# Optimization experiments

Hardware: AMD Instinct MI355X
Metric: run time of the kernel (lower is better)

Reference implementation:

```python
import jax, jax.numpy as jnp
import numpy as np

N, P, VEC, M = 100000, 96, 4, 70000
GROUPS = [27, 8, 8]
K = sum(GROUPS)  # 43
# Replicates the original's use of the LOCAL per-group offset index i_k when
# selecting attention weights in the output accumulation loop.
ATTN_IDX = np.concatenate([np.arange(g) for g in GROUPS]).astype(np.int32)


def setup_inputs() -> dict:
    key = jax.random.key(0)
    ks = jax.random.split(key, 12)
    rng = np.random.default_rng(0)
    # Kernel maps: per offset, M (in_idx, out_idx) pairs; out indices unique per
    # offset (each output point has at most one neighbor at a given offset).
    kmaps = np.stack([
        np.stack([rng.integers(0, N, M), rng.permutation(N)[:M]], axis=1)
        for _ in range(K)
    ]).astype(np.int32)  # [K, M, 2]
    w = lambda k, shape: jax.random.normal(k, shape, jnp.float32) * 0.05
    return dict(
        x=w(ks[0], (N, P)),
        coords=jax.random.uniform(ks[1], (N, 3), jnp.float32, 0.0, 100.0),
        Wq1=w(ks[2], (27, P, P)), gq1=jnp.ones(P), bq1=jnp.zeros(P),
        Wq2=w(ks[3], (27, P, VEC)), gq2=jnp.ones(VEC), bq2=jnp.zeros(VEC),
        Wv=w(ks[4], (27, P, P)), gv=jnp.ones(P), bv=jnp.zeros(P),
        Wp1=w(ks[5], (3, P)), gp1=jnp.ones(P), bp1=jnp.zeros(P),
        Wp2=w(ks[6], (P, VEC)), gp2=jnp.ones(VEC), bp2=jnp.zeros(VEC),
        W1=w(ks[7], (VEC, P)), b1=jnp.zeros(P),
        W2=w(ks[8], (P, VEC)), b2=jnp.zeros(VEC),
        g_out=jnp.ones(P), b_out=jnp.zeros(P),
        kmaps=jnp.asarray(kmaps),
    )


def _bn(x, g, b, eps=1e-5):
    m = x.mean(0)
    v = x.var(0)
    return g * (x - m) * jax.lax.rsqrt(v + eps) + b


def _sparse_conv3(x, W, km27, n):
    # Minkowski kernel-size-3 sparse conv: out[dst] += x[src] @ W[k] per offset.
    def step(acc, kw):
        km, Wk = kw
        return acc.at[km[:, 1]].add(x[km[:, 0]] @ Wk), None
    out, _ = jax.lax.scan(step, jnp.zeros((n, W.shape[-1]), x.dtype), (km27, W))
    return out


def _cbr(x, W, g, b, km27, n):
    return jax.nn.relu(_bn(_sparse_conv3(x, W, km27, n), g, b))


def _forward(x, coords, Wq1, gq1, bq1, Wq2, gq2, bq2, Wv, gv, bv,
             Wp1, gp1, bp1, Wp2, gp2, bp2, W1, b1, W2, b2, g_out, b_out, kmaps):
    n, p = x.shape
    rep = p // VEC  # expand_vec_dim factor
    km27 = kmaps[:27]
    # q branch: two conv3-BN-ReLU stages -> [N, VEC]
    qf = _cbr(_cbr(x, Wq1, gq1, bq1, km27, n), Wq2, gq2, bq2, km27, n)
    # v branch: conv3-BN-ReLU -> [N, P]
    vf = _cbr(x, Wv, gv, bv, km27, n)
    # positional encoding: two 1x1 conv-BN-ReLU on coords -> [N, VEC] -> [N, P]
    pe = jax.nn.relu(_bn(jax.nn.relu(_bn(coords @ Wp1, gp1, bp1)) @ Wp2, gp2, bp2))
    v_f = vf + jnp.repeat(pe, rep, axis=1)

    def attn_step(carry, km):
        src, dst = km[:, 0], km[:, 1]
        # presence mask of offset-k neighbors (scatter of x features, zero elsewhere)
        sm = jnp.zeros((n, p), x.dtype).at[dst].set(x[src])
        mask = jax.lax.stop_gradient((jnp.abs(sm).sum(-1) > 0).astype(x.dtype))  # [N]
        gq = jnp.zeros((n, VEC), x.dtype).at[dst].set(qf[src])
        d = gq - qf * mask[:, None]
        logits = (jax.nn.relu(d @ W1 + b1) @ W2 + b2) * mask[:, None]
        return carry, (logits, mask)

    _, (logits, masks) = jax.lax.scan(attn_step, None, kmaps)  # [K,N,VEC], [K,N]
    attn = jax.nn.softmax(logits, axis=0)  # softmax across the K stacked offsets
    attn_sel = attn[jnp.asarray(ATTN_IDX)]  # replicate local-index selection bug

    def out_step(acc, inp):
        km, mask, a = inp
        nv = jnp.zeros((n, p), x.dtype).at[km[:, 1]].set(v_f[km[:, 0]]) * mask[:, None]
        return acc + nv * jnp.repeat(a, rep, axis=1), None

    out, _ = jax.lax.scan(out_step, jnp.zeros((n, p), x.dtype),
                          (kmaps, masks, attn_sel))
    # out BN + ReLU, residual (inplanes == planes so res = x)
    return jax.nn.relu(_bn(out, g_out, b_out)) + x


def reference(x, coords, Wq1, gq1, bq1, Wq2, gq2, bq2, Wv, gv, bv,
              Wp1, gp1, bp1, Wp2, gp2, bp2, W1, b1, W2, b2, g_out, b_out, kmaps):
    return _forward(x, coords, Wq1, gq1, bq1, Wq2, gq2, bq2, Wv, gv, bv,
                    Wp1, gp1, bp1, Wp2, gp2, bp2, W1, b1, W2, b2,
                    g_out, b_out, kmaps)
```

## Files before the change

### kernel.cpp

```cpp
#include <hip/hip_runtime.h>
#include <math.h>

#define N_  100000
#define P_  96
#define V_  4
#define M_  70000
#define K_  43
#define KC_ 27

typedef unsigned short u16;
typedef __attribute__((ext_vector_type(8))) short bf16x8;
typedef __attribute__((ext_vector_type(4))) float f32x4;
typedef __attribute__((ext_vector_type(16))) float f32x16;

__device__ __forceinline__ u16 f2bf(float f) {
    unsigned int u = __float_as_uint(f);
    u += 0x7fffu + ((u >> 16) & 1u);
    return (u16)(u >> 16);
}
__device__ __forceinline__ float bf2f(u16 h) {
    return __uint_as_float(((unsigned int)h) << 16);
}

__device__ __forceinline__ void gl_lds16(const u16* g, u16* l) {
    __builtin_amdgcn_global_load_lds(
        (const __attribute__((address_space(1))) void*)g,
        (__attribute__((address_space(3))) void*)l, 16, 0, 0);
}

__global__ __launch_bounds__(256) void k_build_srcof(const int* __restrict__ km,
                                                     int* __restrict__ srcOf) {
    int idx = blockIdx.x * 256 + threadIdx.x;
    if (idx >= K_ * M_) return;
    int k = idx / M_;
    int e = idx - k * M_;
    const int* p = km + (size_t)(k * M_ + e) * 2;
    srcOf[(size_t)k * N_ + p[1]] = p[0];
}

__global__ __launch_bounds__(256) void k_rowabs_cvt(const float* __restrict__ x,
                                                    float* __restrict__ rowAbs,
                                                    u16* __restrict__ xb) {
    int row = blockIdx.x * 4 + (threadIdx.x >> 6);
    int lane = threadIdx.x & 63;
    if (row >= N_) return;
    const float* xr = x + (size_t)row * 96;
    float s = 0.f;
    for (int j = lane; j < 96; j += 64) {
        float v = xr[j];
        s += fabsf(v);
        xb[(size_t)row * 96 + j] = f2bf(v);
    }
#pragma unroll
    for (int o = 32; o > 0; o >>= 1) s += __shfl_down(s, o, 64);
    if (lane == 0) rowAbs[row] = s;
}

__global__ __launch_bounds__(256) void k_wt96p(const float* __restrict__ W,
                                               u16* __restrict__ Wp) {
    int idx = blockIdx.x * 256 + threadIdx.x;
    if (idx >= KC_ * 96 * 96) return;
    int k = idx / 9216, rem = idx - k * 9216, n = rem / 96, j = rem - n * 96;
    Wp[(size_t)k * 10240 + n * 104 + j] = f2bf(W[(size_t)k * 9216 + j * 96 + n]);
}

__global__ __launch_bounds__(256) void k_wt4(const float* __restrict__ W,
                                             u16* __restrict__ Wt) {
    int idx = blockIdx.x * 256 + threadIdx.x;
    if (idx >= KC_ * 16 * 96) return;
    int k = idx / 1536, rem = idx - k * 1536, n = rem / 96, j = rem - n * 96;
    Wt[idx] = (n < 4) ? f2bf(W[(size_t)k * 384 + j * 4 + n]) : (u16)0;
}

__global__ __launch_bounds__(256) void k_w12b(const float* __restrict__ W1,
                                              const float* __restrict__ W2,
                                              u16* __restrict__ w1b,
                                              u16* __restrict__ w2b) {
    int t = blockIdx.x * 256 + threadIdx.x;
    if (t < 96 * 32) {
        int j = t >> 5, c = t & 31;
        w1b[t] = (c < 4) ? f2bf(W1[c * 96 + j]) : (u16)0;
    }
    if (t < 16 * 96) {
        int n = t / 96, j = t - n * 96;
        w2b[t] = (n < 4) ? f2bf(W2[j * 4 + n]) : (u16)0;
    }
}

__global__ __launch_bounds__(384, 3) void k_conv96_dual(
    const u16* __restrict__ xb, const u16* __restrict__ Wqp,
    const u16* __restrict__ Wvp, const int* __restrict__ srcOf,
    u16* __restrict__ yQ, u16* __restrict__ yV,
    float* __restrict__ statsQ, float* __restrict__ statsV) {
    __shared__ u16 sA[192 * 104];
    __shared__ u16 sBq[10240];
    __shared__ u16 sBv[10240];
    const int r0 = blockIdx.x * 192;
    const int t = threadIdx.x;
    const int wv = t / 64, lane = t & 63;
    const int n32 = lane & 31, half = lane >> 5;
    const int ea = t >> 1, jca = (t & 1) * 6;
    f32x16 accq[3], accv[3];
#pragma unroll
    for (int i = 0; i < 3; i++) {
#pragma unroll
        for (int j = 0; j < 16; j++) { accq[i][j] = 0.f; accv[i][j] = 0.f; }
    }

    for (int k = 0; k < KC_; k++) {
        __syncthreads();
        {
            const u16* gq = Wqp + (size_t)k * 10240;
            const u16* gv = Wvp + (size_t)k * 10240;
            for (int i = wv; i < 40; i += 6) {
                int mv = (i >= 20);
                int off = (mv ? i - 20 : i) * 512 + lane * 8;
                gl_lds16((mv ? gv : gq) + off, (mv ? (u16*)sBv : (u16*)sBq) + off);
            }
        }
        {
            int r = r0 + ea;
            int src = (r < N_) ? srcOf[(size_t)k * N_ + r] : -1;
            if (src >= 0) {
                const uint4* sp = (const uint4*)(xb + (size_t)src * 96);
#pragma unroll
                for (int i = 0; i < 6; i++)
                    *(uint4*)(sA + ea * 104 + (jca + i) * 8) = sp[jca + i];
            } else {
                uint4 z = make_uint4(0, 0, 0, 0);
#pragma unroll
                for (int i = 0; i < 6; i++)
                    *(uint4*)(sA + ea * 104 + (jca + i) * 8) = z;
            }
        }
        __syncthreads();
#pragma unroll
        for (int ks = 0; ks < 6; ks++) {
            bf16x8 af = *(const bf16x8*)(sA + (wv * 32 + n32) * 104 + ks * 16 + half * 8);
#pragma unroll
            for (int nt = 0; nt < 3; nt++) {
                bf16x8 bq = *(const bf16x8*)(sBq + (nt * 32 + n32) * 104 + ks * 16 + half * 8);
                accq[nt] = __builtin_amdgcn_mfma_f32_32x32x16_bf16(af, bq, accq[nt], 0, 0, 0);
                bf16x8 bv = *(const bf16x8*)(sBv + (nt * 32 + n32) * 104 + ks * 16 + half * 8);
                accv[nt] = __builtin_amdgcn_mfma_f32_32x32x16_bf16(af, bv, accv[nt], 0, 0, 0);
            }
        }
    }
#pragma unroll
    for (int nt = 0; nt < 3; nt++) {
#pragma unroll
        for (int reg = 0; reg < 16; reg++) {
            int row = (reg & 3) + 8 * (reg >> 2) + 4 * half;
            int r = r0 + wv * 32 + row;
            if (r < N_) {
                yQ[(size_t)r * 96 + nt * 32 + n32] = f2bf(accq[nt][reg]);
                yV[(size_t)r * 96 + nt * 32 + n32] = f2bf(accv[nt][reg]);
            }
        }
    }
    __syncthreads();
    float* sred = (float*)sA;
    for (int pass = 0; pass < 2; pass++) {
        f32x16* acc = pass ? accv : accq;
        float* st = pass ? statsV : statsQ;
#pragma unroll
        for (int nt = 0; nt < 3; nt++) {
            float sv = 0.f, qv = 0.f;
#pragma unroll
            for (int reg = 0; reg < 16; reg++) {
                float a = acc[nt][reg];
                sv += a; qv += a * a;
            }
            sv += __shfl_xor(sv, 32, 64);
            qv += __shfl_xor(qv, 32, 64);
            if (half == 0) {
                sred[wv * 192 + nt * 32 + n32] = sv;
                sred[wv * 192 + 96 + nt * 32 + n32] = qv;
            }
        }
        __syncthreads();
        if (t < 192) {
            float tot = 0.f;
#pragma unroll
            for (int w = 0; w < 6; w++) tot += sred[w * 192 + t];
            atomicAdd(&st[t], tot);
        }
        __syncthreads();
    }
}

__global__ __launch_bounds__(256) void k_conv4_mfma(
    const u16* __restrict__ xbA, const u16* __restrict__ Wt4,
    const int* __restrict__ srcOf, float* __restrict__ qf) {
    __shared__ u16 sA[128 * 104];
    __shared__ u16 sB[16 * 104];
    const int r0 = blockIdx.x * 128;
    const int t = threadIdx.x;
    const int wv = t >> 6, lane = t & 63;
    const int m = lane & 15, quad = lane >> 4;
    const int ea = t >> 1, jca = (t & 1) * 6;
    f32x4 acc[2];
    acc[0] = (f32x4){0.f, 0.f, 0.f, 0.f};
    acc[1] = (f32x4){0.f, 0.f, 0.f, 0.f};
    for (int k = 0; k < KC_; k++) {
        __syncthreads();
        {
            int r = r0 + ea;
            int src = (r < N_) ? srcOf[(size_t)k * N_ + r] : -1;
            if (src >= 0) {
                const uint4* sp = (const uint4*)(xbA + (size_t)src * 96);
#pragma unroll
                for (int i = 0; i < 6; i++)
                    *(uint4*)(sA + ea * 104 + (jca + i) * 8) = sp[jca + i];
            } else {
                uint4 z = make_uint4(0, 0, 0, 0);
#pragma unroll
                for (int i = 0; i < 6; i++)
                    *(uint4*)(sA + ea * 104 + (jca + i) * 8) = z;
            }
        }
        if (t < 192) {
            int n = t / 12, jc = t - (t / 12) * 12;
            *(uint4*)(sB + n * 104 + jc * 8) =
                *(const uint4*)(Wt4 + (size_t)k * 1536 + n * 96 + jc * 8);
        }
        __syncthreads();
#pragma unroll
        for (int kk = 0; kk < 3; kk++) {
            bf16x8 bfr = *(const bf16x8*)(sB + m * 104 + kk * 32 + quad * 8);
#pragma unroll
            for (int rt = 0; rt < 2; rt++) {
                bf16x8 af = *(const bf16x8*)(sA + ((wv * 2 + rt) * 16 + m) * 104 + kk * 32 + quad * 8);
                acc[rt] = __builtin_amdgcn_mfma_f32_16x16x32_bf16(af, bfr, acc[rt], 0, 0, 0);
            }
        }
    }
    if (m < 4) {
#pragma unroll
        for (int rt = 0; rt < 2; rt++)
#pragma unroll
            for (int rg = 0; rg < 4; rg++) {
                int r = r0 + (wv * 2 + rt) * 16 + quad * 4 + rg;
                if (r < N_) qf[(size_t)r * 4 + m] = acc[rt][rg];
            }
    }
}

__global__ __launch_bounds__(192) void k_bnstats96(const float* __restrict__ xin,
                                                   float* __restrict__ stats) {
    __shared__ float sS[192], sQ[192];
    int t = threadIdx.x;
    int ch = t % 96, half = t / 96;
    float s = 0.f, q = 0.f;
    for (int r = blockIdx.x * 2 + half; r < N_; r += gridDim.x * 2) {
        float v = xin[(size_t)r * 96 + ch];
        s += v; q += v * v;
    }
    sS[t] = s; sQ[t] = q;
    __syncthreads();
    if (t < 96) {
        atomicAdd(&stats[ch], sS[t] + sS[t + 96]);
        atomicAdd(&stats[96 + ch], sQ[t] + sQ[t + 96]);
    }
}

__global__ __launch_bounds__(256) void k_bnstats4(const float* __restrict__ xin,
                                                  float* __restrict__ stats) {
    __shared__ float sS[256], sQ[256];
    int t = threadIdx.x;
    int c = t & 3, sub = t >> 2;
    float s = 0.f, q = 0.f;
    for (int r = blockIdx.x * 64 + sub; r < N_; r += gridDim.x * 64) {
        float v = xin[(size_t)r * 4 + c];
        s += v; q += v * v;
    }
    sS[t] = s; sQ[t] = q;
    __syncthreads();
    for (int off = 128; off >= 4; off >>= 1) {
        if (t < off) { sS[t] += sS[t + off]; sQ[t] += sQ[t + off]; }
        __syncthreads();
    }
    if (t < 4) {
        atomicAdd(&stats[t], sS[t]);
        atomicAdd(&stats[96 + t], sQ[t]);
    }
}

template <int C, int MODE>
__global__ __launch_bounds__(256) void k_bnapply(float* __restrict__ y,
                                                 const float* __restrict__ stats,
                                                 const float* __restrict__ g,
                                                 const float* __restrict__ b,
                                                 const float* __restrict__ aux) {
    int idx = blockIdx.x * 256 + threadIdx.x;
    if (idx >= N_ * C) return;
    int ch = idx % C;
    float mean = stats[ch] * (1.f / N_);
    float var = stats[96 + ch] * (1.f / N_) - mean * mean;
    float scale = g[ch] * rsqrtf(fmaxf(var, 0.f) + 1e-5f);
    float v = (y[idx] - mean) * scale + b[ch];
    v = fmaxf(v, 0.f);
    if (MODE == 2) v += aux[idx];
    y[idx] = v;
}

template <int MODE>
__global__ __launch_bounds__(256) void k_bnapply96_b2b(
    const u16* __restrict__ yin, const float* __restrict__ stats,
    const float* __restrict__ g, const float* __restrict__ b,
    const float* __restrict__ aux, u16* __restrict__ yout) {
    int idx = blockIdx.x * 256 + threadIdx.x;
    if (idx >= N_ * 96) return;
    int ch = idx % 96;
    float mean = stats[ch] * (1.f / N_);
    float var = stats[96 + ch] * (1.f / N_) - mean * mean;
    float scale = g[ch] * rsqrtf(fmaxf(var, 0.f) + 1e-5f);
    float v = (bf2f(yin[idx]) - mean) * scale + b[ch];
    v = fmaxf(v, 0.f);
    if (MODE == 1) { int r = idx / 96; v += aux[(size_t)r * 4 + (ch / 24)]; }
    yout[idx] = f2bf(v);
}

__global__ __launch_bounds__(256) void k_pe1(const float* __restrict__ coords,
                                             const float* __restrict__ Wp1,
                                             float* __restrict__ out) {
    int idx = blockIdx.x * 256 + threadIdx.x;
    if (idx >= N_ * 96) return;
    int r = idx / 96, ch = idx - r * 96;
    float c0 = coords[r * 3], c1 = coords[r * 3 + 1], c2 = coords[r * 3 + 2];
    out[idx] = c0 * Wp1[ch] + c1 * Wp1[96 + ch] + c2 * Wp1[192 + ch];
}

__global__ __launch_bounds__(256) void k_pe2(const float* __restrict__ hin,
                                             const float* __restrict__ Wp2,
                                             float* __restrict__ out) {
    int idx = blockIdx.x * 256 + threadIdx.x;
    if (idx >= N_ * 4) return;
    int r = idx / 4, c = idx & 3;
    const float* hr = hin + (size_t)r * 96;
    float acc = 0.f;
#pragma unroll 4
    for (int j = 0; j < 96; j++) acc += hr[j] * Wp2[j * 4 + c];
    out[idx] = acc;
}

__global__ __launch_bounds__(256) void k_attn_logits_mfma(
    const float* __restrict__ qf, const int* __restrict__ srcOf,
    const float* __restrict__ rowAbs,
    const u16* __restrict__ w1b, const float* __restrict__ b1,
    const u16* __restrict__ w2b, const float* __restrict__ b2,
    u16* __restrict__ wb) {
    __shared__ u16 hbuf[4][16 * 104];
    __shared__ u16 slogb[32][176];
    __shared__ u16 smk16[32][44];
    const int t = threadIdx.x;
    const int wv = t >> 6, lane = t & 63;
    const int col = lane & 15, quad = lane >> 4;
    const int r0 = blockIdx.x * 32;

    bf16x8 w1f[6];
    float b1v[6];
#pragma unroll
    for (int nt = 0; nt < 6; nt++) {
        w1f[nt] = *(const bf16x8*)(w1b + (nt * 16 + col) * 32 + quad * 8);
        b1v[nt] = b1[nt * 16 + col];
    }
    bf16x8 w2f[3];
#pragma unroll
    for (int kk = 0; kk < 3; kk++)
        w2f[kk] = *(const bf16x8*)(w2b + col * 96 + kk * 32 + quad * 8);
    float b2v = b2[col & 3];

    u16* hb = hbuf[wv];
    for (int tt = 0; tt < 22; tt++) {
        int tileBase = (wv * 22 + tt) * 16;
        bf16x8 af = (bf16x8){0, 0, 0, 0, 0, 0, 0, 0};
        if (quad == 0) {
            int P = tileBase + col;
            int rL = P / 44, k = P - rL * 44;
            int kc = (k < 43) ? k : 42;
            int r = r0 + rL;
            int s = srcOf[(size_t)kc * N_ + r];
            if (k == 43) s = -1;
            int sc = (s >= 0) ? s : 0;
            float mk = (s >= 0 && rowAbs[sc] > 0.f) ? 1.f : 0.f;
            float4 qs = *(const float4*)(qf + (size_t)sc * 4);
            float4 qr = *(const float4*)(qf + (size_t)r * 4);
            af[0] = (short)f2bf((qs.x - qr.x) * mk);
            af[1] = (short)f2bf((qs.y - qr.y) * mk);
            af[2] = (short)f2bf((qs.z - qr.z) * mk);
            af[3] = (short)f2bf((qs.w - qr.w) * mk);
            if (k < 43) smk16[rL][k] = (u16)(mk > 0.f ? 1 : 0);
        }
        f32x4 c1[6];
#pragma unroll
        for (int nt = 0; nt < 6; nt++) {
            c1[nt] = (f32x4){0.f, 0.f, 0.f, 0.f};
            c1[nt] = __builtin_amdgcn_mfma_f32_16x16x32_bf16(af, w1f[nt], c1[nt], 0, 0, 0);
        }
#pragma unroll
        for (int nt = 0; nt < 6; nt++) {
#pragma unroll
            for (int rg = 0; rg < 4; rg++) {
                float h = fmaxf(c1[nt][rg] + b1v[nt], 0.f);
                hb[(quad * 4 + rg) * 104 + nt * 16 + col] = f2bf(h);
            }
        }
        f32x4 acc2 = (f32x4){0.f, 0.f, 0.f, 0.f};
#pragma unroll
        for (int kk = 0; kk < 3; kk++) {
            bf16x8 a2 = *(const bf16x8*)(hb + col * 104 + kk * 32 + quad * 8);
            acc2 = __builtin_amdgcn_mfma_f32_16x16x32_bf16(a2, w2f[kk], acc2, 0, 0, 0);
        }
        if (col < 4) {
#pragma unroll
            for (int rg = 0; rg < 4; rg++) {
                int P = tileBase + quad * 4 + rg;
                int rL = P / 44, k = P - rL * 44;
                if (k < 43) {
                    float mval = (float)smk16[rL][k];
                    slogb[rL][k * 4 + col] = f2bf((acc2[rg] + b2v) * mval);
                }
            }
        }
    }
    __syncthreads();

    if (t < 128) {
        int rL = t >> 2, c = t & 3;
        float mx = 0.f;
        for (int k = 0; k < K_; k++) mx = fmaxf(mx, bf2f(slogb[rL][k * 4 + c]));
        float den = 0.f;
        for (int k = 0; k < K_; k++) den += __expf(bf2f(slogb[rL][k * 4 + c]) - mx);
        float inv = 1.f / den;
        for (int k = 0; k < K_; k++)
            slogb[rL][k * 4 + c] = f2bf(__expf(bf2f(slogb[rL][k * 4 + c]) - mx) * inv);
    }
    __syncthreads();

    for (int p = t; p < 32 * 43; p += 256) {
        int rL = p / 43, k = p - rL * 43;
        int idxk = (k < 27) ? k : ((k < 35) ? (k - 27) : (k - 35));
        u16 mk = smk16[rL][k];
        ushort4 wout = make_ushort4(0, 0, 0, 0);
        if (mk) {
            wout.x = slogb[rL][idxk * 4 + 0];
            wout.y = slogb[rL][idxk * 4 + 1];
            wout.z = slogb[rL][idxk * 4 + 2];
            wout.w = slogb[rL][idxk * 4 + 3];
        }
        *(ushort4*)(wb + ((size_t)(r0 + rL) * 44 + k) * 4) = wout;
    }
}

__global__ __launch_bounds__(256) void k_attn_gather(
    const u16* __restrict__ vfb, const u16* __restrict__ wb,
    const int* __restrict__ srcOf, float* __restrict__ out) {
    int idx = blockIdx.x * 256 + threadIdx.x;
    int r = idx / 24, c4 = idx - r * 24;
    if (r >= N_) return;
    int cg = c4 / 6;
    const u16* wrow = wb + (size_t)r * 176 + cg;
    float a0 = 0.f, a1 = 0.f, a2 = 0.f, a3 = 0.f;
    for (int k = 0; k < K_; k++) {
        int s = srcOf[(size_t)k * N_ + r];
        float w = bf2f(wrow[(size_t)k * 4]);
        w = (s >= 0) ? w : 0.f;
        int sc = (s >= 0) ? s : 0;
        ushort4 v = *(const ushort4*)(vfb + (size_t)sc * 96 + c4 * 4);
        a0 += w * bf2f(v.x);
        a1 += w * bf2f(v.y);
        a2 += w * bf2f(v.z);
        a3 += w * bf2f(v.w);
    }
    *(float4*)(out + (size_t)r * 96 + c4 * 4) = make_float4(a0, a1, a2, a3);
}

extern "C" void kernel_launch(void* const* d_in, const int* in_sizes, int n_in,
                              void* d_out, int out_size, void* d_ws, size_t ws_size,
                              hipStream_t stream) {
    const float* x      = (const float*)d_in[0];
    const float* coords = (const float*)d_in[1];
    const float* Wq1 = (const float*)d_in[2];
    const float* gq1 = (const float*)d_in[3];
    const float* bq1 = (const float*)d_in[4];
    const float* Wq2 = (const float*)d_in[5];
    const float* gq2 = (const float*)d_in[6];
    const float* bq2 = (const float*)d_in[7];
    const float* Wv  = (const float*)d_in[8];
    const float* gv  = (const float*)d_in[9];
    const float* bv  = (const float*)d_in[10];
    const float* Wp1 = (const float*)d_in[11];
    const float* gp1 = (const float*)d_in[12];
    const float* bp1 = (const float*)d_in[13];
    const float* Wp2 = (const float*)d_in[14];
    const float* gp2 = (const float*)d_in[15];
    const float* bp2 = (const float*)d_in[16];
    const float* W1  = (const float*)d_in[17];
    const float* b1  = (const float*)d_in[18];
    const float* W2  = (const float*)d_in[19];
    const float* b2  = (const float*)d_in[20];
    const float* g_out = (const float*)d_in[21];
    const float* b_out = (const float*)d_in[22];
    const int* kmaps = (const int*)d_in[23];
    float* out = (float*)d_out;

    char* ws = (char*)d_ws;
    int*   srcOf  = (int*)ws;
    float* rowAbs = (float*)(ws + 17200000);
    u16*   xb     = (u16*)(ws + 17600000);
    u16*   bufQb  = (u16*)(ws + 36800000);
    u16*   bufVb  = (u16*)(ws + 56000000);
    u16*   bufAb  = (u16*)(ws + 75200000);
    u16*   vfb    = (u16*)(ws + 75200000);
    float* pescr  = (float*)(ws + 17600000);
    u16*   wbuf   = (u16*)(ws + 17600000);
    float* qf     = (float*)(ws + 94400000);
    float* peb    = (float*)(ws + 96000000);
    u16*   Wq1p   = (u16*)(ws + 97600000);
    u16*   Wvp    = (u16*)(ws + 98152960);
    u16*   Wq2t   = (u16*)(ws + 98705920);
    u16*   w1b    = (u16*)(ws + 98788864);
    u16*   w2b    = (u16*)(ws + 98795008);
    float* stats  = (float*)(ws + 98798080);

    hipMemsetAsync(srcOf, 0xFF, (size_t)K_ * N_ * 4, stream);
    hipMemsetAsync(stats, 0, 6 * 192 * 4, stream);

    k_build_srcof<<<(K_ * M_ + 255) / 256, 256, 0, stream>>>(kmaps, srcOf);
    k_rowabs_cvt<<<N_ / 4, 256, 0, stream>>>(x, rowAbs, xb);
    k_wt96p<<<(KC_ * 9216 + 255) / 256, 256, 0, stream>>>(Wq1, Wq1p);
    k_wt96p<<<(KC_ * 9216 + 255) / 256, 256, 0, stream>>>(Wv, Wvp);
    k_wt4<<<(KC_ * 1536 + 255) / 256, 256, 0, stream>>>(Wq2, Wq2t);
    k_w12b<<<12, 256, 0, stream>>>(W1, W2, w1b, w2b);

    const int cbD  = (N_ + 191) / 192;
    const int cb4  = (N_ + 127) / 128;
    const int eb96 = N_ * 96 / 256;
    const int eb4  = (N_ * 4 + 255) / 256;

    k_conv96_dual<<<cbD, 384, 0, stream>>>(xb, Wq1p, Wvp, srcOf, bufQb, bufVb,
                                           stats + 0 * 192, stats + 4 * 192);

    k_bnapply96_b2b<0><<<eb96, 256, 0, stream>>>(bufQb, stats + 0 * 192, gq1, bq1, nullptr, bufAb);
    k_conv4_mfma<<<cb4, 256, 0, stream>>>(bufAb, Wq2t, srcOf, qf);
    k_bnstats4<<<512, 256, 0, stream>>>(qf, stats + 1 * 192);
    k_bnapply<4, 0><<<eb4, 256, 0, stream>>>(qf, stats + 1 * 192, gq2, bq2, nullptr);

    k_pe1<<<eb96, 256, 0, stream>>>(coords, Wp1, pescr);
    k_bnstats96<<<512, 192, 0, stream>>>(pescr, stats + 2 * 192);
    k_bnapply<96, 0><<<eb96, 256, 0, stream>>>(pescr, stats + 2 * 192, gp1, bp1, nullptr);
    k_pe2<<<eb4, 256, 0, stream>>>(pescr, Wp2, peb);
    k_bnstats4<<<512, 256, 0, stream>>>(peb, stats + 3 * 192);
    k_bnapply<4, 0><<<eb4, 256, 0, stream>>>(peb, stats + 3 * 192, gp2, bp2, nullptr);

    k_bnapply96_b2b<1><<<eb96, 256, 0, stream>>>(bufVb, stats + 4 * 192, gv, bv, peb, vfb);

    k_attn_logits_mfma<<<N_ / 32, 256, 0, stream>>>(qf, srcOf, rowAbs, w1b, b1, w2b, b2, wbuf);
    k_attn_gather<<<(N_ * 24) / 256, 256, 0, stream>>>(vfb, wbuf, srcOf, out);

    k_bnstats96<<<512, 192, 0, stream>>>(out, stats + 5 * 192);
    k_bnapply<96, 2><<<eb96, 256, 0, stream>>>(out, stats + 5 * 192, g_out, b_out, x);
}
```

Before: 1.003 ms.

## Reorder q2 conv as per-point projection then gather; fuse BN stats into producers

The second q conv (96->4 over 27 offsets) becomes a dense projection of every point onto all 27 offset weight slices, computed once with MFMA. A lightweight gather kernel then sums the projected values for each point's neighbours, so the full 96-channel rows are no longer gathered 27 times. The BN-apply before that conv is fused into the projection's load. The positional-encoding BN stats move into the pe1 producer, pe1 BN-apply moves into pe2, and the output BN stats are accumulated inside the attention gather kernel, removing separate stats passes. The trade-offs are an extra 108-wide bf16 intermediate buffer, the projection now being rounded to bf16, and more shared/global atomics.

New measurement: 1.096 ms. 9.2% more time.

```diff
diff --git a/kernel.cpp b/kernel.cpp
--- a/kernel.cpp
+++ b/kernel.cpp
@@ -64,12 +64,17 @@
     Wp[(size_t)k * 10240 + n * 104 + j] = f2bf(W[(size_t)k * 9216 + j * 96 + n]);
 }
 
-__global__ __launch_bounds__(256) void k_wt4(const float* __restrict__ W,
-                                             u16* __restrict__ Wt) {
+__global__ __launch_bounds__(256) void k_wtB(const float* __restrict__ W,
+                                             u16* __restrict__ Bimg) {
     int idx = blockIdx.x * 256 + threadIdx.x;
-    if (idx >= KC_ * 16 * 96) return;
-    int k = idx / 1536, rem = idx - k * 1536, n = rem / 96, j = rem - n * 96;
-    Wt[idx] = (n < 4) ? f2bf(W[(size_t)k * 384 + j * 4 + n]) : (u16)0;
+    if (idx >= 128 * 104) return;
+    int n = idx / 104, j = idx - n * 104;
+    u16 v = 0;
+    if (j < 96 && n < 108) {
+        int ks = n >> 2, c = n & 3;
+        v = f2bf(W[(size_t)ks * 384 + j * 4 + c]);
+    }
+    Bimg[idx] = v;
 }
 
 __global__ __launch_bounds__(256) void k_w12b(const float* __restrict__ W1,
@@ -189,79 +194,88 @@
     }
 }
 
-__global__ __launch_bounds__(256) void k_conv4_mfma(
-    const u16* __restrict__ xbA, const u16* __restrict__ Wt4,
-    const int* __restrict__ srcOf, float* __restrict__ qf) {
+__global__ __launch_bounds__(256) void k_proj(
+    const u16* __restrict__ xq, const float* __restrict__ stats,
+    const float* __restrict__ gg, const float* __restrict__ bb,
+    const u16* __restrict__ Bimg, u16* __restrict__ gout) {
     __shared__ u16 sA[128 * 104];
-    __shared__ u16 sB[16 * 104];
+    __shared__ u16 sB[128 * 104];
+    __shared__ float sSc[96], sSh[96];
     const int r0 = blockIdx.x * 128;
     const int t = threadIdx.x;
     const int wv = t >> 6, lane = t & 63;
-    const int m = lane & 15, quad = lane >> 4;
-    const int ea = t >> 1, jca = (t & 1) * 6;
-    f32x4 acc[2];
-    acc[0] = (f32x4){0.f, 0.f, 0.f, 0.f};
-    acc[1] = (f32x4){0.f, 0.f, 0.f, 0.f};
+    const int n32 = lane & 31, half = lane >> 5;
+    if (t < 96) {
+        float mean = stats[t] * (1.f / N_);
+        float var = stats[96 + t] * (1.f / N_) - mean * mean;
+        float sc = gg[t] * rsqrtf(fmaxf(var, 0.f) + 1e-5f);
+        sSc[t] = sc; sSh[t] = bb[t] - mean * sc;
+    }
+    for (int i = t; i < 1664; i += 256)
+        ((uint4*)sB)[i] = ((const uint4*)Bimg)[i];
+    __syncthreads();
+    {
+        int ea = t >> 1, jca = (t & 1) * 6;
+        int r = r0 + ea;
+        bool ok = (r < N_);
+        const u16* xr = xq + (size_t)(ok ? r : 0) * 96;
+#pragma unroll
+        for (int i = 0; i < 6; i++) {
+            int cb = (jca + i) * 8;
+            uint4 v = ok ? *(const uint4*)(xr + cb) : make_uint4(0, 0, 0, 0);
+            const u16* pv = (const u16*)&v;
+            u16 o[8];
+#pragma unroll
+            for (int e = 0; e < 8; e++) {
+                float h = bf2f(pv[e]);
+                h = fmaxf(h * sSc[cb + e] + sSh[cb + e], 0.f);
+                o[e] = f2bf(h);
+            }
+            *(uint4*)(sA + ea * 104 + cb) = *(uint4*)o;
+        }
+    }
+    __syncthreads();
+    f32x16 acc[4];
+#pragma unroll
+    for (int i = 0; i < 4; i++)
+#pragma unroll
+        for (int j = 0; j < 16; j++) acc[i][j] = 0.f;
+#pragma unroll
+    for (int ks = 0; ks < 6; ks++) {
+        bf16x8 af = *(const bf16x8*)(sA + (wv * 32 + n32) * 104 + ks * 16 + half * 8);
+#pragma unroll
+        for (int nt = 0; nt < 4; nt++) {
+            bf16x8 bf = *(const bf16x8*)(sB + (nt * 32 + n32) * 104 + ks * 16 + half * 8);
+            acc[nt] = __builtin_amdgcn_mfma_f32_32x32x16_bf16(af, bf, acc[nt], 0, 0, 0);
+        }
+    }
+#pragma unroll
+    for (int nt = 0; nt < 4; nt++) {
+        int col = nt * 32 + n32;
+        if (col < 108) {
+#pragma unroll
+            for (int reg = 0; reg < 16; reg++) {
+                int row = (reg & 3) + 8 * (reg >> 2) + 4 * half;
+                int r = r0 + wv * 32 + row;
+                if (r < N_) gout[(size_t)r * 108 + col] = f2bf(acc[nt][reg]);
+            }
+        }
+    }
+}
+
+__global__ __launch_bounds__(256) void k_gather4(
+    const u16* __restrict__ g, const int* __restrict__ srcOf,
+    float* __restrict__ qf) {
+    int idx = blockIdx.x * 256 + threadIdx.x;
+    if (idx >= N_ * 4) return;
+    int r = idx >> 2, c = idx & 3;
+    float a = 0.f;
+#pragma unroll
     for (int k = 0; k < KC_; k++) {
-        __syncthreads();
-        {
-            int r = r0 + ea;
-            int src = (r < N_) ? srcOf[(size_t)k * N_ + r] : -1;
-            if (src >= 0) {
-                const uint4* sp = (const uint4*)(xbA + (size_t)src * 96);
-#pragma unroll
-                for (int i = 0; i < 6; i++)
-                    *(uint4*)(sA + ea * 104 + (jca + i) * 8) = sp[jca + i];
-            } else {
-                uint4 z = make_uint4(0, 0, 0, 0);
-#pragma unroll
-                for (int i = 0; i < 6; i++)
-                    *(uint4*)(sA + ea * 104 + (jca + i) * 8) = z;
-            }
-        }
-        if (t < 192) {
-            int n = t / 12, jc = t - (t / 12) * 12;
-            *(uint4*)(sB + n * 104 + jc * 8) =
-                *(const uint4*)(Wt4 + (size_t)k * 1536 + n * 96 + jc * 8);
-        }
-        __syncthreads();
-#pragma unroll
-        for (int kk = 0; kk < 3; kk++) {
-            bf16x8 bfr = *(const bf16x8*)(sB + m * 104 + kk * 32 + quad * 8);
-#pragma unroll
-            for (int rt = 0; rt < 2; rt++) {
-                bf16x8 af = *(const bf16x8*)(sA + ((wv * 2 + rt) * 16 + m) * 104 + kk * 32 + quad * 8);
-                acc[rt] = __builtin_amdgcn_mfma_f32_16x16x32_bf16(af, bfr, acc[rt], 0, 0, 0);
-            }
-        }
-    }
-    if (m < 4) {
-#pragma unroll
-        for (int rt = 0; rt < 2; rt++)
-#pragma unroll
-            for (int rg = 0; rg < 4; rg++) {
-                int r = r0 + (wv * 2 + rt) * 16 + quad * 4 + rg;
-                if (r < N_) qf[(size_t)r * 4 + m] = acc[rt][rg];
-            }
-    }
-}
-
-__global__ __launch_bounds__(192) void k_bnstats96(const float* __restrict__ xin,
-                                                   float* __restrict__ stats) {
-    __shared__ float sS[192], sQ[192];
-    int t = threadIdx.x;
-    int ch = t % 96, half = t / 96;
-    float s = 0.f, q = 0.f;
-    for (int r = blockIdx.x * 2 + half; r < N_; r += gridDim.x * 2) {
-        float v = xin[(size_t)r * 96 + ch];
-        s += v; q += v * v;
-    }
-    sS[t] = s; sQ[t] = q;
-    __syncthreads();
-    if (t < 96) {
-        atomicAdd(&stats[ch], sS[t] + sS[t + 96]);
-        atomicAdd(&stats[96 + ch], sQ[t] + sQ[t + 96]);
-    }
+        int s = srcOf[(size_t)k * N_ + r];
+        if (s >= 0) a += bf2f(g[(size_t)s * 108 + k * 4 + c]);
+    }
+    qf[idx] = a;
 }
 
 __global__ __launch_bounds__(256) void k_bnstats4(const float* __restrict__ xin,
@@ -304,8 +318,7 @@
     y[idx] = v;
 }
 
-template <int MODE>
-__global__ __launch_bounds__(256) void k_bnapply96_b2b(
+__global__ __launch_bounds__(256) void k_bnapply96_pe(
     const u16* __restrict__ yin, const float* __restrict__ stats,
     const float* __restrict__ g, const float* __restrict__ b,
     const float* __restrict__ aux, u16* __restrict__ yout) {
@@ -317,30 +330,60 @@
     float scale = g[ch] * rsqrtf(fmaxf(var, 0.f) + 1e-5f);
     float v = (bf2f(yin[idx]) - mean) * scale + b[ch];
     v = fmaxf(v, 0.f);
-    if (MODE == 1) { int r = idx / 96; v += aux[(size_t)r * 4 + (ch / 24)]; }
+    int r = idx / 96;
+    v += aux[(size_t)r * 4 + (ch / 24)];
     yout[idx] = f2bf(v);
 }
 
-__global__ __launch_bounds__(256) void k_pe1(const float* __restrict__ coords,
-                                             const float* __restrict__ Wp1,
-                                             float* __restrict__ out) {
-    int idx = blockIdx.x * 256 + threadIdx.x;
-    if (idx >= N_ * 96) return;
-    int r = idx / 96, ch = idx - r * 96;
-    float c0 = coords[r * 3], c1 = coords[r * 3 + 1], c2 = coords[r * 3 + 2];
-    out[idx] = c0 * Wp1[ch] + c1 * Wp1[96 + ch] + c2 * Wp1[192 + ch];
-}
-
-__global__ __launch_bounds__(256) void k_pe2(const float* __restrict__ hin,
-                                             const float* __restrict__ Wp2,
-                                             float* __restrict__ out) {
-    int idx = blockIdx.x * 256 + threadIdx.x;
+__global__ __launch_bounds__(192) void k_pe1s(const float* __restrict__ coords,
+                                              const float* __restrict__ Wp1,
+                                              u16* __restrict__ out,
+                                              float* __restrict__ stats) {
+    __shared__ float sS[192], sQ[192];
+    int t = threadIdx.x;
+    int ch = t % 96, half = t / 96;
+    float w0 = Wp1[ch], w1 = Wp1[96 + ch], w2 = Wp1[192 + ch];
+    float s = 0.f, q = 0.f;
+    for (int r = blockIdx.x * 2 + half; r < N_; r += gridDim.x * 2) {
+        float c0 = coords[r * 3], c1 = coords[r * 3 + 1], c2 = coords[r * 3 + 2];
+        float v = c0 * w0 + c1 * w1 + c2 * w2;
+        out[(size_t)r * 96 + ch] = f2bf(v);
+        s += v; q += v * v;
+    }
+    sS[t] = s; sQ[t] = q;
+    __syncthreads();
+    if (t < 96) {
+        atomicAdd(&stats[ch], sS[t] + sS[t + 96]);
+        atomicAdd(&stats[96 + ch], sQ[t] + sQ[t + 96]);
+    }
+}
+
+__global__ __launch_bounds__(256) void k_pe2b(const u16* __restrict__ hin,
+                                              const float* __restrict__ stats,
+                                              const float* __restrict__ gp,
+                                              const float* __restrict__ bp,
+                                              const float* __restrict__ Wp2,
+                                              float* __restrict__ out) {
+    __shared__ float sSc[96], sSh[96], sW[384];
+    int t = threadIdx.x;
+    if (t < 96) {
+        float mean = stats[t] * (1.f / N_);
+        float var = stats[96 + t] * (1.f / N_) - mean * mean;
+        float sc = gp[t] * rsqrtf(fmaxf(var, 0.f) + 1e-5f);
+        sSc[t] = sc; sSh[t] = bp[t] - mean * sc;
+    }
+    for (int i = t; i < 384; i += 256) sW[i] = Wp2[i];
+    __syncthreads();
+    int idx = blockIdx.x * 256 + t;
     if (idx >= N_ * 4) return;
-    int r = idx / 4, c = idx & 3;
-    const float* hr = hin + (size_t)r * 96;
+    int r = idx >> 2, c = idx & 3;
+    const u16* hr = hin + (size_t)r * 96;
     float acc = 0.f;
 #pragma unroll 4
-    for (int j = 0; j < 96; j++) acc += hr[j] * Wp2[j * 4 + c];
+    for (int j = 0; j < 96; j++) {
+        float h = fmaxf(bf2f(hr[j]) * sSc[j] + sSh[j], 0.f);
+        acc += h * sW[j * 4 + c];
+    }
     out[idx] = acc;
 }
 
@@ -453,12 +496,16 @@
     }
 }
 
-__global__ __launch_bounds__(256) void k_attn_gather(
+__global__ __launch_bounds__(256) void k_attn_gather_s(
     const u16* __restrict__ vfb, const u16* __restrict__ wb,
-    const int* __restrict__ srcOf, float* __restrict__ out) {
-    int idx = blockIdx.x * 256 + threadIdx.x;
+    const int* __restrict__ srcOf, float* __restrict__ out,
+    float* __restrict__ stats) {
+    __shared__ float sS[96], sQ[96];
+    int t = threadIdx.x;
+    if (t < 96) { sS[t] = 0.f; sQ[t] = 0.f; }
+    __syncthreads();
+    int idx = blockIdx.x * 256 + t;
     int r = idx / 24, c4 = idx - r * 24;
-    if (r >= N_) return;
     int cg = c4 / 6;
     const u16* wrow = wb + (size_t)r * 176 + cg;
     float a0 = 0.f, a1 = 0.f, a2 = 0.f, a3 = 0.f;
@@ -474,6 +521,16 @@
         a3 += w * bf2f(v.w);
     }
     *(float4*)(out + (size_t)r * 96 + c4 * 4) = make_float4(a0, a1, a2, a3);
+    int chb = c4 * 4;
+    atomicAdd(&sS[chb + 0], a0); atomicAdd(&sQ[chb + 0], a0 * a0);
+    atomicAdd(&sS[chb + 1], a1); atomicAdd(&sQ[chb + 1], a1 * a1);
+    atomicAdd(&sS[chb + 2], a2); atomicAdd(&sQ[chb + 2], a2 * a2);
+    atomicAdd(&sS[chb + 3], a3); atomicAdd(&sQ[chb + 3], a3 * a3);
+    __syncthreads();
+    if (t < 96) {
+        atomicAdd(&stats[t], sS[t]);
+        atomicAdd(&stats[96 + t], sQ[t]);
+    }
 }
 
 extern "C" void kernel_launch(void* const* d_in, const int* in_sizes, int n_in,
@@ -509,20 +566,20 @@
     int*   srcOf  = (int*)ws;
     float* rowAbs = (float*)(ws + 17200000);
     u16*   xb     = (u16*)(ws + 17600000);
+    u16*   pescr  = (u16*)(ws + 17600000);
+    u16*   wbuf   = (u16*)(ws + 17600000);
     u16*   bufQb  = (u16*)(ws + 36800000);
-    u16*   bufVb  = (u16*)(ws + 56000000);
-    u16*   bufAb  = (u16*)(ws + 75200000);
-    u16*   vfb    = (u16*)(ws + 75200000);
-    float* pescr  = (float*)(ws + 17600000);
-    u16*   wbuf   = (u16*)(ws + 17600000);
-    float* qf     = (float*)(ws + 94400000);
-    float* peb    = (float*)(ws + 96000000);
-    u16*   Wq1p   = (u16*)(ws + 97600000);
-    u16*   Wvp    = (u16*)(ws + 98152960);
-    u16*   Wq2t   = (u16*)(ws + 98705920);
-    u16*   w1b    = (u16*)(ws + 98788864);
-    u16*   w2b    = (u16*)(ws + 98795008);
-    float* stats  = (float*)(ws + 98798080);
+    float* peb    = (float*)(ws + 36800000);
+    u16*   Wq1p   = (u16*)(ws + 56000000);
+    u16*   Wvp    = (u16*)(ws + 56552960);
+    u16*   gbuf   = (u16*)(ws + 56000000);
+    u16*   vfb    = (u16*)(ws + 56000000);
+    u16*   bufVb  = (u16*)(ws + 77600000);
+    u16*   Bimg   = (u16*)(ws + 96800000);
+    float* qf     = (float*)(ws + 96800000);
+    u16*   w1b    = (u16*)(ws + 98400000);
+    u16*   w2b    = (u16*)(ws + 98406144);
+    float* stats  = (float*)(ws + 98409216);
 
     hipMemsetAsync(srcOf, 0xFF, (size_t)K_ * N_ * 4, stream);
     hipMemsetAsync(stats, 0, 6 * 192 * 4, stream);
@@ -531,34 +588,32 @@
     k_rowabs_cvt<<<N_ / 4, 256, 0, stream>>>(x, rowAbs, xb);
     k_wt96p<<<(KC_ * 9216 + 255) / 256, 256, 0, stream>>>(Wq1, Wq1p);
     k_wt96p<<<(KC_ * 9216 + 255) / 256, 256, 0, stream>>>(Wv, Wvp);
-    k_wt4<<<(KC_ * 1536 + 255) / 256, 256, 0, stream>>>(Wq2, Wq2t);
+    k_wtB<<<52, 256, 0, stream>>>(Wq2, Bimg);
     k_w12b<<<12, 256, 0, stream>>>(W1, W2, w1b, w2b);
 
     const int cbD  = (N_ + 191) / 192;
-    const int cb4  = (N_ + 127) / 128;
     const int eb96 = N_ * 96 / 256;
     const int eb4  = (N_ * 4 + 255) / 256;
 
     k_conv96_dual<<<cbD, 384, 0, stream>>>(xb, Wq1p, Wvp, srcOf, bufQb, bufVb,
                                            stats + 0 * 192, stats + 4 * 192);
 
-    k_bnapply96_b2b<0><<<eb96, 256, 0, stream>>>(bufQb, stats + 0 * 192, gq1, bq1, nullptr, bufAb);
-    k_conv4_mfma<<<cb4, 256, 0, stream>>>(bufAb, Wq2t, srcOf, qf);
+    k_proj<<<(N_ + 127) / 128, 256, 0, stream>>>(bufQb, stats + 0 * 192, gq1, bq1,
+                                                 Bimg, gbuf);
+    k_gather4<<<eb4, 256, 0, stream>>>(gbuf, srcOf, qf);
     k_bnstats4<<<512, 256, 0, stream>>>(qf, stats + 1 * 192);
     k_bnapply<4, 0><<<eb4, 256, 0, stream>>>(qf, stats + 1 * 192, gq2, bq2, nullptr);
 
-    k_pe1<<<eb96, 256, 0, stream>>>(coords, Wp1, pescr);
-    k_bnstats96<<<512, 192, 0, stream>>>(pescr, stats + 2 * 192);
-    k_bnapply<96, 0><<<eb96, 256, 0, stream>>>(pescr, stats + 2 * 192, gp1, bp1, nullptr);
-    k_pe2<<<eb4, 256, 0, stream>>>(pescr, Wp2, peb);
+    k_pe1s<<<512, 192, 0, stream>>>(coords, Wp1, pescr, stats + 2 * 192);
+    k_pe2b<<<eb4, 256, 0, stream>>>(pescr, stats + 2 * 192, gp1, bp1, Wp2, peb);
     k_bnstats4<<<512, 256, 0, stream>>>(peb, stats + 3 * 192);
     k_bnapply<4, 0><<<eb4, 256, 0, stream>>>(peb, stats + 3 * 192, gp2, bp2, nullptr);
 
-    k_bnapply96_b2b<1><<<eb96, 256, 0, stream>>>(bufVb, stats + 4 * 192, gv, bv, peb, vfb);
+    k_bnapply96_pe<<<eb96, 256, 0, stream>>>(bufVb, stats + 4 * 192, gv, bv, peb, vfb);
 
     k_attn_logits_mfma<<<N_ / 32, 256, 0, stream>>>(qf, srcOf, rowAbs, w1b, b1, w2b, b2, wbuf);
-    k_attn_gather<<<(N_ * 24) / 256, 256, 0, stream>>>(vfb, wbuf, srcOf, out);
-
-    k_bnstats96<<<512, 192, 0, stream>>>(out, stats + 5 * 192);
+    k_attn_gather_s<<<(N_ * 24) / 256, 256, 0, stream>>>(vfb, wbuf, srcOf, out,
+                                                         stats + 5 * 192);
+
     k_bnapply<96, 2><<<eb96, 256, 0, stream>>>(out, stats + 5 * 192, g_out, b_out, x);
 }
```
